# Kernel optimization log

Measured on AMD Instinct MI355X. Metric: run time of the kernel, lower is better.

## Reference

```python
import jax, jax.numpy as jnp
from jax import lax
import numpy as np

D = 128      # d_model
DI = 256     # d_inner = expand * d_model
NS = 16      # d_state
R = 8        # dt_rank = ceil(d_model/16)
DC = 4       # d_conv
B, C, N, P = 4, 32, 6, 64
T = N * P
RATIOS = (1, 3, 6)
OUT = 768


def _ln(x, g, b):
    m = x.mean(-1, keepdims=True)
    v = ((x - m) ** 2).mean(-1, keepdims=True)
    return (x - m) * lax.rsqrt(v + 1e-5) * g + b


def _event_order(n_base):
    # chronological interleaving of multi-band tokens (static, python-level)
    events = []
    for step in range(1, n_base + 1):
        for k, r in enumerate(RATIOS):
            if step % r == 0:
                events.append((k, step // r - 1))
    nk = [n_base // r for r in RATIOS]
    offs = np.cumsum([0] + nk[:-1])
    return np.array([offs[k] + w for k, w in events], dtype=np.int32)


def setup_inputs():
    key = jax.random.key(0)
    ks = iter(jax.random.split(key, 64))
    def nrm(shape, std):
        return jax.random.normal(next(ks), shape, jnp.float32) * std
    inp = {}
    inp['x'] = jax.random.normal(next(ks), (B, C, N, P), jnp.float32)
    inp['perm'] = jax.random.randint(next(ks), (B, C), 0, C)
    # sample_proj: Conv1d(1,D,7,pad=3) -> GELU -> Conv1d(D,D,1)
    inp['sp_w1'] = nrm((D, 1, 7), 0.3)
    inp['sp_b1'] = jnp.zeros((D,))
    inp['sp_w2'] = nrm((D, D, 1), D ** -0.5)
    inp['sp_b2'] = jnp.zeros((D,))
    nb = 4  # fwd0, fwd1, bwd0, bwd1 mamba blocks (stacked)
    inp['ln_g'] = jnp.ones((nb, D)); inp['ln_b'] = jnp.zeros((nb, D))
    inp['W_in'] = nrm((nb, D, 2 * DI), D ** -0.5)
    inp['conv_w'] = nrm((nb, DI, DC), DC ** -0.5)
    inp['conv_b'] = jnp.zeros((nb, DI))
    inp['W_x'] = nrm((nb, DI, R + 2 * NS), DI ** -0.5)
    inp['W_dt'] = nrm((nb, R, DI), R ** -0.5)
    inp['b_dt'] = jnp.full((nb, DI), -4.6) + nrm((nb, DI), 0.1)
    inp['A_log'] = jnp.broadcast_to(jnp.log(jnp.arange(1, NS + 1, dtype=jnp.float32)), (nb, DI, NS)) + 0.0
    inp['Dp'] = jnp.ones((nb, DI))
    inp['W_out'] = nrm((nb, DI, D), DI ** -0.5)
    inp['b_out'] = jnp.zeros((nb, D))
    inp['fuse_w'] = nrm((2 * D, D), (2 * D) ** -0.5); inp['fuse_b'] = jnp.zeros((D,))
    inp['band_emb'] = nrm((3, D), 0.02)
    inp['band_pw'] = nrm((3, D, D), D ** -0.5); inp['band_pb'] = jnp.zeros((3, D))
    inp['pos_w'] = nrm((D, 1, 19, 7), (19 * 7) ** -0.5); inp['pos_b'] = jnp.zeros((D,))
    inp['hemi_w'] = nrm((2 * D, D), (2 * D) ** -0.5); inp['hemi_b'] = jnp.zeros((D,))
    Lf = sum(N // r for r in RATIOS) * D  # flatten_dim = 9*128
    inp['a_ln_g'] = jnp.ones((Lf,)); inp['a_ln_b'] = jnp.zeros((Lf,))
    inp['a_w1'] = nrm((Lf, 200), Lf ** -0.5); inp['a_b1'] = jnp.zeros((200,))
    inp['a_w2'] = nrm((200, 1), 200 ** -0.5); inp['a_b2'] = jnp.zeros((1,))
    inp['m_ln_g'] = jnp.ones((Lf,)); inp['m_ln_b'] = jnp.zeros((Lf,))
    inp['m_w1'] = nrm((Lf, 1024), Lf ** -0.5); inp['m_b1'] = jnp.zeros((1024,))
    inp['m_w2'] = nrm((1024, OUT), 1024 ** -0.5); inp['m_b2'] = jnp.zeros((OUT,))
    return inp


def _mamba(h, lng, lnb, Win, cw, cb, Wx, Wdt, bdt, Alog, Dpar, Wout, bout):
    # pre-norm residual Mamba block: h + Mamba(LN(h))
    x = _ln(h, lng, lnb)
    xz = x @ Win                      # (BC,T,2*DI)
    xp, z = jnp.split(xz, 2, axis=-1)
    xt = xp.swapaxes(1, 2)            # (BC,DI,T)
    xt = lax.conv_general_dilated(xt, cw[:, None, :], (1,), [(DC - 1, 0)],
                                  dimension_numbers=('NCH', 'OIH', 'NCH'),
                                  feature_group_count=DI) + cb[None, :, None]
    xc = jax.nn.silu(xt).swapaxes(1, 2)   # (BC,T,DI)
    xdbl = xc @ Wx
    dt = jax.nn.softplus(xdbl[..., :R] @ Wdt + bdt)   # (BC,T,DI)
    Bs = xdbl[..., R:R + NS]
    Cs = xdbl[..., R + NS:]
    A = -jnp.exp(Alog)                # (DI,NS)
    def step(hc, inp):
        x_t, dt_t, b_t, c_t = inp
        hc = hc * jnp.exp(dt_t[..., None] * A) + (dt_t * x_t)[..., None] * b_t[:, None, :]
        return hc, jnp.einsum('bdn,bn->bd', hc, c_t)
    h0 = jnp.zeros((xc.shape[0], DI, NS), xc.dtype)
    _, ys = lax.scan(step, h0, (xc.swapaxes(0, 1), dt.swapaxes(0, 1),
                                Bs.swapaxes(0, 1), Cs.swapaxes(0, 1)))
    y = ys.swapaxes(0, 1) + xc * Dpar
    y = y * jax.nn.silu(z)
    return h + y @ Wout + bout


def reference(x, perm, sp_w1, sp_b1, sp_w2, sp_b2, ln_g, ln_b, W_in, conv_w, conv_b,
              W_x, W_dt, b_dt, A_log, Dp, W_out, b_out, fuse_w, fuse_b, band_emb,
              band_pw, band_pb, pos_w, pos_b, hemi_w, hemi_b, a_ln_g, a_ln_b,
              a_w1, a_b1, a_w2, a_b2, m_ln_g, m_ln_b, m_w1, m_b1, m_w2, m_b2):
    Bq, Cq, Nq, Pq = x.shape
    Tq = Nq * Pq
    ts = x.reshape(Bq * Cq, 1, Tq)
    # sample_proj
    f = lax.conv_general_dilated(ts, sp_w1, (1,), [(3, 3)],
                                 dimension_numbers=('NCH', 'OIH', 'NCH')) + sp_b1[None, :, None]
    f = jax.nn.gelu(f)
    f = jnp.einsum('bct,oc->bot', f, sp_w2[:, :, 0]) + sp_b2[None, :, None]
    h = f.swapaxes(1, 2)              # (BC,T,D)
    # bidirectional mamba stack
    hf = h
    for i in range(2):
        hf = _mamba(hf, ln_g[i], ln_b[i], W_in[i], conv_w[i], conv_b[i], W_x[i],
                    W_dt[i], b_dt[i], A_log[i], Dp[i], W_out[i], b_out[i])
    hb = h[:, ::-1]
    for i in range(2, 4):
        hb = _mamba(hb, ln_g[i], ln_b[i], W_in[i], conv_w[i], conv_b[i], W_x[i],
                    W_dt[i], b_dt[i], A_log[i], Dp[i], W_out[i], b_out[i])
    hb = hb[:, ::-1]
    feats = jnp.concatenate([hf, hb], -1) @ fuse_w + fuse_b   # (BC,T,D)
    # multi-band token extraction (end-of-period samples)
    band = []
    for k, r in enumerate(RATIOS):
        p = Pq * r
        nk = Tq // p
        pos = jnp.arange(nk) * p + (p - 1)
        band.append(feats[:, pos] @ band_pw[k] + band_pb[k] + band_emb[k])
    flat = jnp.concatenate(band, axis=1)
    toks = flat[:, jnp.asarray(_event_order(Nq))]   # chronological interleave, (BC,L,D)
    L = toks.shape[1]
    t = toks.reshape(Bq, Cq, L, D).transpose(0, 3, 1, 2)   # (B,D,C,L)
    pe = lax.conv_general_dilated(t, pos_w, (1, 1), [(9, 9), (3, 3)],
                                  dimension_numbers=('NCHW', 'OIHW', 'NCHW'),
                                  feature_group_count=D) + pos_b[None, :, None, None]
    t = (t + pe).transpose(0, 2, 3, 1)              # (B,C,L,D)
    # hemispheric channel gather + fuse
    tf = jnp.take_along_axis(t, perm[:, :, None, None], axis=1)
    fused = jnp.concatenate([t, tf], -1) @ hemi_w + hemi_b
    flatf = fused.reshape(Bq, Cq, L * D)
    # attention-MLP semantic readout
    logits = (jax.nn.gelu(_ln(flatf, a_ln_g, a_ln_b) @ a_w1 + a_b1) @ a_w2 + a_b2)[..., 0]
    w = jax.nn.softmax(logits, -1)
    agg = jnp.einsum('bcf,bc->bf', flatf, w)
    return jax.nn.gelu(_ln(agg, m_ln_g, m_ln_b) @ m_w1 + m_b1) @ m_w2 + m_b2
```

## Files before the change

kernel.cpp:

```cpp
#include <hip/hip_runtime.h>


typedef unsigned short u16;
using bf16x8 = __attribute__((ext_vector_type(8))) short;
using f32x4  = __attribute__((ext_vector_type(4))) float;

#define TT    384
#define BCn   128
#define TOKn  49152
#define CH3   64
#define NCH3  (TT/CH3)

__device__ __forceinline__ float b2f(u16 u) {
  return __uint_as_float(((unsigned)u) << 16);
}
__device__ __forceinline__ u16 f2b(float f) {
  unsigned u = __float_as_uint(f);
  u += 0x7fffu + ((u >> 16) & 1u);
  return (u16)(u >> 16);
}
__device__ __forceinline__ float gelu_t(float x) {
  float u2 = 1.5957691216057308f * (x + 0.044715f * x * x * x);
  float e = __expf(u2);
  float th = 1.f - 2.f / (e + 1.f);
  return 0.5f * x * (1.f + th);
}
__device__ __forceinline__ float silu_f(float x) { return x / (1.f + __expf(-x)); }
__device__ __forceinline__ float softplus_f(float x) {
  return fmaxf(x, 0.f) + __logf(1.f + __expf(-fabsf(x)));
}

__device__ __forceinline__ float dpp_xor1(float v) {
  return __int_as_float(__builtin_amdgcn_mov_dpp(
      __float_as_int(v), 0xB1 , 0xF, 0xF, true));
}
__device__ __forceinline__ float dpp_xor2(float v) {
  return __int_as_float(__builtin_amdgcn_mov_dpp(
      __float_as_int(v), 0x4E , 0xF, 0xF, true));
}

__device__ __forceinline__ float block_sum(float v, float* sb) {
  #pragma unroll
  for (int m = 32; m; m >>= 1) v += __shfl_xor(v, m);
  int lane = threadIdx.x & 63, wid = threadIdx.x >> 6;
  if (lane == 0) sb[wid] = v;
  __syncthreads();
  float tot = sb[0] + sb[1] + sb[2] + sb[3];
  __syncthreads();
  return tot;
}

template <int EPI, int KT>
__global__ __launch_bounds__(256) void k_mm(
    const u16* __restrict__ X, const u16* __restrict__ WT,
    const float* __restrict__ bias, int Nw, int rev,
    float* __restrict__ o0, u16* __restrict__ ob0) {
  constexpr int AK = KT + 8;
  __shared__ u16 As[64 * AK];
  __shared__ u16 Bs[64 * AK];
  const int tid = threadIdx.x;
  const int tok0 = blockIdx.x * 64;
  const int n0 = blockIdx.y * 64;

  constexpr int VPR = KT / 8;
  constexpr int ITER = 64 * VPR / 256;
  #pragma unroll
  for (int j = 0; j < ITER; ++j) {
    int idx = tid + j * 256;
    int row = idx / VPR, vec = idx % VPR;
    *reinterpret_cast<uint4*>(&As[row * AK + vec * 8]) =
        *reinterpret_cast<const uint4*>(&X[(size_t)(tok0 + row) * KT + vec * 8]);
    *reinterpret_cast<uint4*>(&Bs[row * AK + vec * 8]) =
        *reinterpret_cast<const uint4*>(&WT[(size_t)(n0 + row) * KT + vec * 8]);
  }
  __syncthreads();

  const int w = tid >> 6, lane = tid & 63;
  const int wm = (w & 1) * 32, wn = (w >> 1) * 32;
  const int lrow = lane & 15, quad = lane >> 4;
  f32x4 acc[2][2] = {};
  #pragma unroll
  for (int ks = 0; ks < KT / 32; ++ks) {
    int koff = ks * 32 + quad * 8;
    bf16x8 a0 = *reinterpret_cast<const bf16x8*>(&As[(wm + lrow) * AK + koff]);
    bf16x8 a1 = *reinterpret_cast<const bf16x8*>(&As[(wm + 16 + lrow) * AK + koff]);
    bf16x8 b0 = *reinterpret_cast<const bf16x8*>(&Bs[(wn + lrow) * AK + koff]);
    bf16x8 b1 = *reinterpret_cast<const bf16x8*>(&Bs[(wn + 16 + lrow) * AK + koff]);
    acc[0][0] = __builtin_amdgcn_mfma_f32_16x16x32_bf16(a0, b0, acc[0][0], 0, 0, 0);
    acc[0][1] = __builtin_amdgcn_mfma_f32_16x16x32_bf16(a0, b1, acc[0][1], 0, 0, 0);
    acc[1][0] = __builtin_amdgcn_mfma_f32_16x16x32_bf16(a1, b0, acc[1][0], 0, 0, 0);
    acc[1][1] = __builtin_amdgcn_mfma_f32_16x16x32_bf16(a1, b1, acc[1][1], 0, 0, 0);
  }

  #pragma unroll
  for (int mi = 0; mi < 2; ++mi)
    #pragma unroll
    for (int ni = 0; ni < 2; ++ni)
      #pragma unroll
      for (int r = 0; r < 4; ++r) {
        int tok = tok0 + wm + mi * 16 + quad * 4 + r;
        int n = n0 + wn + ni * 16 + lrow;
        float v = acc[mi][ni][r];
        if (EPI == 0) {
          v += bias[n];
          int bc = tok / TT, t = tok % TT;
          int tok2 = rev ? (bc * TT + (TT - 1 - t)) : tok;
          o0[(size_t)tok2 * 128 + n] = v;
        } else if (EPI == 1) {
          ob0[(size_t)tok * 512 + n] = f2b(v);
        } else if (EPI == 2) {
          if (n < 40) o0[(size_t)tok * 40 + n] = v;
        } else if (EPI == 3) {
          v += bias[n];
          o0[(size_t)tok * 128 + n] += v;
        }
      }
  (void)Nw;
}

__global__ __launch_bounds__(256) void k_tin(const float* __restrict__ W,
                                             u16* __restrict__ WT) {
  int i = blockIdx.x * 256 + threadIdx.x;
  int blk = i >> 16, r = i & 65535;
  int n = r >> 7, k = r & 127;
  WT[i] = f2b(W[blk * 65536 + k * 512 + n]);
}
__global__ __launch_bounds__(256) void k_tout(const float* __restrict__ W,
                                              u16* __restrict__ WT) {
  int i = blockIdx.x * 256 + threadIdx.x;
  int blk = i >> 15, r = i & 32767;
  int n = r >> 8, k = r & 255;
  WT[i] = f2b(W[blk * 32768 + k * 128 + n]);
}
__global__ __launch_bounds__(256) void k_tx(const float* __restrict__ W,
                                            u16* __restrict__ WT) {
  int i = blockIdx.x * 256 + threadIdx.x;
  int blk = i >> 14, r = i & 16383;
  int n = r >> 8, k = r & 255;
  WT[i] = (n < 40) ? f2b(W[blk * 10240 + k * 40 + n]) : 0;
}
__global__ __launch_bounds__(256) void k_tsp(const float* __restrict__ W,
                                             u16* __restrict__ WT) {
  int i = blockIdx.x * 256 + threadIdx.x;
  WT[i] = f2b(W[i]);
}

__global__ __launch_bounds__(256) void k_spec1(const float* __restrict__ x,
                                               const float* __restrict__ w1,
                                               const float* __restrict__ b1,
                                               u16* __restrict__ F) {
  __shared__ float xs[70];
  __shared__ float wsh[128 * 7];
  __shared__ float bs[128];
  int bc = blockIdx.x / 6, tile = blockIdx.x % 6;
  int tid = threadIdx.x;
  for (int i = tid; i < 896; i += 256) wsh[i] = w1[i];
  if (tid < 128) bs[tid] = b1[tid];
  int t0 = tile * 64;
  if (tid < 70) {
    int t = t0 - 3 + tid;
    xs[tid] = (t >= 0 && t < TT) ? x[(size_t)bc * TT + t] : 0.f;
  }
  __syncthreads();
  #pragma unroll
  for (int k = 0; k < 32; ++k) {
    int idx = tid + k * 256;
    int tl = idx >> 7, c = idx & 127;
    const float* wr = &wsh[c * 7];
    float acc = bs[c];
    #pragma unroll
    for (int j = 0; j < 7; ++j) acc += xs[tl + j] * wr[j];
    F[((size_t)(bc * TT + t0 + tl)) * 128 + c] = f2b(gelu_t(acc));
  }
}

__global__ __launch_bounds__(256) void k_ln(const float* __restrict__ H,
                                            const float* __restrict__ gg,
                                            const float* __restrict__ bb,
                                            u16* __restrict__ XLN) {
  int tid = threadIdx.x;
  int lane = tid & 63, wid = tid >> 6;
  int token = blockIdx.x * 4 + wid;
  const float* hr = H + (size_t)token * 128;
  float a = hr[lane], b = hr[lane + 64];
  float s = a + b;
  #pragma unroll
  for (int m = 32; m; m >>= 1) s += __shfl_xor(s, m);
  float mean = s * (1.f / 128.f);
  float d1 = a - mean, d2 = b - mean;
  float q = d1 * d1 + d2 * d2;
  #pragma unroll
  for (int m = 32; m; m >>= 1) q += __shfl_xor(q, m);
  float rs = rsqrtf(q * (1.f / 128.f) + 1e-5f);
  XLN[(size_t)token * 128 + lane] = f2b(d1 * rs * gg[lane] + bb[lane]);
  XLN[(size_t)token * 128 + lane + 64] =
      f2b(d2 * rs * gg[lane + 64] + bb[lane + 64]);
}

__global__ __launch_bounds__(256) void k_conv(const u16* __restrict__ XZ,
                                              const float* __restrict__ cw,
                                              const float* __restrict__ cb,
                                              u16* __restrict__ XC) {
  int idx = blockIdx.x * 256 + threadIdx.x;
  int d4 = idx & 63;
  int tokg = idx >> 6;
  int t = tokg % TT;
  int dbase = d4 * 4;
  const float* cwp = cw + dbase * 4;
  float wv[4][4];
  #pragma unroll
  for (int j = 0; j < 4; ++j)
    #pragma unroll
    for (int k = 0; k < 4; ++k) wv[j][k] = cwp[j * 4 + k];
  float accv[4];
  #pragma unroll
  for (int j = 0; j < 4; ++j) accv[j] = cb[dbase + j];
  #pragma unroll
  for (int k = 0; k < 4; ++k) {
    int tt = t + k - 3;
    if (tt < 0) continue;
    ushort4 xv = *reinterpret_cast<const ushort4*>(
        &XZ[(size_t)(tokg + k - 3) * 512 + dbase]);
    u16 xa[4];
    *reinterpret_cast<ushort4*>(xa) = xv;
    #pragma unroll
    for (int j = 0; j < 4; ++j) accv[j] += b2f(xa[j]) * wv[j][k];
  }
  u16 oa[4];
  #pragma unroll
  for (int j = 0; j < 4; ++j) oa[j] = f2b(silu_f(accv[j]));
  *reinterpret_cast<ushort4*>(&XC[(size_t)tokg * 256 + dbase]) =
      *reinterpret_cast<ushort4*>(oa);
}

__global__ __launch_bounds__(256) void k_scan(
    const float* __restrict__ XDBL, u16* __restrict__ XC,
    const u16* __restrict__ XZ, const float* __restrict__ Wdt,
    const float* __restrict__ bdt, const float* __restrict__ Alog,
    const float* __restrict__ Dpv) {
  __shared__ float xdl[CH3 * 40];
  __shared__ float dtl[CH3 * 64];
  __shared__ u16   xcl[CH3 * 64];
  __shared__ u16   ybuf[CH3 * 64];
  const int tid = threadIdx.x;
  const int bc = blockIdx.x >> 2, dq = blockIdx.x & 3;
  const int ng = tid & 3;
  const int dl = tid >> 2;
  const int dcol = tid & 63;

  const int d_scan = dq * 64 + dl;
  float A[4];
  #pragma unroll
  for (int j = 0; j < 4; ++j)
    A[j] = -__expf(Alog[d_scan * 16 + ng * 4 + j]);
  float wdtr[8];
  #pragma unroll
  for (int j = 0; j < 8; ++j) wdtr[j] = Wdt[j * 256 + dq * 64 + dcol];
  const float bd = bdt[dq * 64 + dcol];
  const float dpar = Dpv[dq * 64 + dcol];

  const size_t base = (size_t)bc * TT;
  const float* xdg = XDBL + base * 40;
  const uint4* xcu4 = (const uint4*)XC;

  float sx[10];
  uint4 scx[2];
  auto issue_loads = [&](int c) {
    const float* p = xdg + (size_t)c * CH3 * 40;
    #pragma unroll
    for (int k = 0; k < 10; ++k) sx[k] = p[tid + k * 256];
    #pragma unroll
    for (int k = 0; k < 2; ++k) {
      int v = tid + k * 256;
      int t = v >> 3, q = v & 7;
      size_t tok = base + (size_t)c * CH3 + t;
      scx[k] = xcu4[tok * 32 + dq * 8 + q];
    }
  };
  auto write_lds = [&]() {
    #pragma unroll
    for (int k = 0; k < 10; ++k) xdl[tid + k * 256] = sx[k];
    #pragma unroll
    for (int k = 0; k < 2; ++k) {
      int v = tid + k * 256;
      ((uint4*)xcl)[v] = scx[k];
    }
  };

  issue_loads(0);
  write_lds();
  __syncthreads();

  float hc[4] = {};
  for (int c = 0; c < NCH3; ++c) {
    if (c + 1 < NCH3) issue_loads(c + 1);
    #pragma unroll
    for (int k = 0; k < 16; ++k) {
      int t = (tid >> 6) + 4 * k;
      float4 x0 = *reinterpret_cast<const float4*>(&xdl[t * 40]);
      float4 x1 = *reinterpret_cast<const float4*>(&xdl[t * 40 + 4]);
      float acc = bd;
      acc += x0.x * wdtr[0] + x0.y * wdtr[1] + x0.z * wdtr[2] + x0.w * wdtr[3];
      acc += x1.x * wdtr[4] + x1.y * wdtr[5] + x1.z * wdtr[6] + x1.w * wdtr[7];
      dtl[t * 64 + dcol] = softplus_f(acc);
    }
    __syncthreads();
    #pragma unroll 4
    for (int t = 0; t < CH3; ++t) {
      float dtv = dtl[t * 64 + dl];
      float xcv = b2f(xcl[t * 64 + dl]);
      float4 Bv = *reinterpret_cast<const float4*>(&xdl[t * 40 + 8 + ng * 4]);
      float4 Cv = *reinterpret_cast<const float4*>(&xdl[t * 40 + 24 + ng * 4]);
      float dx = dtv * xcv;
      float e0 = __expf(A[0] * dtv);
      float e1 = __expf(A[1] * dtv);
      float e2 = __expf(A[2] * dtv);
      float e3 = __expf(A[3] * dtv);
      hc[0] = fmaf(hc[0], e0, dx * Bv.x);
      hc[1] = fmaf(hc[1], e1, dx * Bv.y);
      hc[2] = fmaf(hc[2], e2, dx * Bv.z);
      hc[3] = fmaf(hc[3], e3, dx * Bv.w);
      float yv = hc[0] * Cv.x + hc[1] * Cv.y + hc[2] * Cv.z + hc[3] * Cv.w;
      yv += dpp_xor1(yv);
      yv += dpp_xor2(yv);
      if (ng == 0) ybuf[t * 64 + dl] = f2b(yv);
    }
    __syncthreads();
    #pragma unroll
    for (int k = 0; k < 16; ++k) {
      int t = (tid >> 6) + 4 * k;
      int v = t * 64 + dcol;
      size_t tok = base + (size_t)c * CH3 + t;
      float y = b2f(ybuf[v]);
      float xcv = b2f(xcl[v]);
      float zz = b2f(XZ[tok * 512 + 256 + dq * 64 + dcol]);
      y = (y + xcv * dpar) * silu_f(zz);
      XC[tok * 256 + dq * 64 + dcol] = f2b(y);
    }
    __syncthreads();
    if (c + 1 < NCH3) {
      write_lds();
      __syncthreads();
    }
  }
}

__global__ __launch_bounds__(256) void k_gather(const float* __restrict__ H,
                                                float* __restrict__ XF,
                                                int half, int revpos) {
  int i = blockIdx.x * 256 + threadIdx.x;
  int col = i & 127, row = i >> 7;
  int bc = row / 6, u = row % 6;
  int tu = 63 + 64 * u;
  int t = revpos ? (TT - 1 - tu) : tu;
  XF[(size_t)row * 256 + half + col] = H[(size_t)(bc * TT + t) * 128 + col];
}

__global__ __launch_bounds__(128) void k_fuse(const float* __restrict__ XF,
                                              const float* __restrict__ fw,
                                              const float* __restrict__ fb,
                                              float* __restrict__ FE) {
  int row = blockIdx.x;
  int d = threadIdx.x;
  __shared__ float rows[256];
  rows[d] = XF[(size_t)row * 256 + d];
  rows[128 + d] = XF[(size_t)row * 256 + 128 + d];
  __syncthreads();
  float acc = fb[d];
  for (int k = 0; k < 256; ++k) acc += rows[k] * fw[k * 128 + d];
  FE[(size_t)row * 128 + d] = acc;
}

__global__ __launch_bounds__(128) void k_band(const float* __restrict__ FE,
                                              const float* __restrict__ pw,
                                              const float* __restrict__ pb,
                                              const float* __restrict__ pe,
                                              float* __restrict__ TO) {
  const int u_of[9] = {0, 1, 2, 2, 3, 4, 5, 5, 5};
  const int k_of[9] = {0, 0, 0, 1, 0, 0, 0, 1, 2};
  int bid = blockIdx.x;
  int bc = bid / 9, j = bid % 9;
  int u = u_of[j], kq = k_of[j];
  __shared__ float fs[128];
  int d = threadIdx.x;
  fs[d] = FE[(size_t)(bc * 6 + u) * 128 + d];
  __syncthreads();
  float acc = pb[kq * 128 + d] + pe[kq * 128 + d];
  const float* wp = pw + kq * 16384 + d;
  for (int c = 0; c < 128; ++c) acc += fs[c] * wp[c * 128];
  TO[(size_t)bid * 128 + d] = acc;
}

__global__ __launch_bounds__(256) void k_pos(const float* __restrict__ TO,
                                             const float* __restrict__ pw,
                                             const float* __restrict__ pb,
                                             float* __restrict__ T2) {
  int idx = blockIdx.x * 256 + threadIdx.x;
  int d = idx & 127;
  int l = (idx >> 7) % 9;
  int c = (idx / 1152) & 31;
  int b = idx / 36864;
  float acc = 0.f;
  const float* wd = pw + d * 133;
  for (int i = 0; i < 19; ++i) {
    int ci = c + i - 9;
    if (ci < 0 || ci >= 32) continue;
    const float* trow = TO + (size_t)(b * 32 + ci) * 9 * 128 + d;
    #pragma unroll
    for (int jj = 0; jj < 7; ++jj) {
      int lj = l + jj - 3;
      if (lj < 0 || lj >= 9) continue;
      acc += trow[lj * 128] * wd[i * 7 + jj];
    }
  }
  T2[idx] = TO[idx] + acc + pb[d];
}

__global__ __launch_bounds__(128) void k_hemi(const float* __restrict__ T2,
                                              const int* __restrict__ perm,
                                              const float* __restrict__ hw,
                                              const float* __restrict__ hb,
                                              float* __restrict__ FL) {
  int bid = blockIdx.x;
  int b = bid / 288;
  int c = (bid / 9) % 32;
  int l = bid % 9;
  int pc = perm[b * 32 + c];
  __shared__ float rows[256];
  int d = threadIdx.x;
  rows[d] = T2[((size_t)(b * 32 + c) * 9 + l) * 128 + d];
  rows[128 + d] = T2[((size_t)(b * 32 + pc) * 9 + l) * 128 + d];
  __syncthreads();
  float acc = hb[d];
  for (int k = 0; k < 256; ++k) acc += rows[k] * hw[k * 128 + d];
  FL[(size_t)(b * 32 + c) * 1152 + l * 128 + d] = acc;
}

__global__ __launch_bounds__(256) void k_attn(
    const float* __restrict__ FL, const float* __restrict__ lg,
    const float* __restrict__ lb, const float* __restrict__ w1,
    const float* __restrict__ b1, const float* __restrict__ w2,
    const float* __restrict__ ab2, float* __restrict__ LO) {
  __shared__ float xn[1152];
  __shared__ float sb[4];
  int row = blockIdx.x;
  int tid = threadIdx.x;
  const float* xr = FL + (size_t)row * 1152;
  float xl[5];
  int cnt = 0;
  float s = 0.f;
  for (int i = tid; i < 1152; i += 256) { xl[cnt] = xr[i]; s += xl[cnt]; ++cnt; }
  float tot = block_sum(s, sb);
  float mean = tot * (1.f / 1152.f);
  float q = 0.f;
  for (int k = 0; k < cnt; ++k) { float dd = xl[k] - mean; q += dd * dd; }
  float qt = block_sum(q, sb);
  float rs = rsqrtf(qt * (1.f / 1152.f) + 1e-5f);
  cnt = 0;
  for (int i = tid; i < 1152; i += 256) {
    xn[i] = (xl[cnt] - mean) * rs * lg[i] + lb[i];
    ++cnt;
  }
  __syncthreads();
  float g = 0.f;
  if (tid < 200) {
    float acc = b1[tid];
    for (int i = 0; i < 1152; ++i) acc += xn[i] * w1[i * 200 + tid];
    g = gelu_t(acc);
  }
  __syncthreads();
  if (tid < 200) xn[tid] = g;
  __syncthreads();
  float s2 = (tid < 200) ? xn[tid] * w2[tid] : 0.f;
  float t2 = block_sum(s2, sb);
  if (tid == 0) LO[row] = t2 + ab2[0];
}

__global__ __launch_bounds__(256) void k_smagg(const float* __restrict__ FL,
                                               const float* __restrict__ LO,
                                               float* __restrict__ AG) {
  int b = blockIdx.x;
  int tid = threadIdx.x;
  __shared__ float w[32];
  if (tid == 0) {
    float mx = -1e30f;
    for (int c = 0; c < 32; ++c) mx = fmaxf(mx, LO[b * 32 + c]);
    float sum = 0.f;
    for (int c = 0; c < 32; ++c) { float e = __expf(LO[b * 32 + c] - mx); w[c] = e; sum += e; }
    float inv = 1.f / sum;
    for (int c = 0; c < 32; ++c) w[c] *= inv;
  }
  __syncthreads();
  for (int f = tid; f < 1152; f += 256) {
    float acc = 0.f;
    for (int c = 0; c < 32; ++c) acc += FL[(size_t)(b * 32 + c) * 1152 + f] * w[c];
    AG[b * 1152 + f] = acc;
  }
}

__global__ __launch_bounds__(256) void k_lnm(const float* __restrict__ AG,
                                             const float* __restrict__ lg,
                                             const float* __restrict__ lb,
                                             float* __restrict__ AGN) {
  __shared__ float sb[4];
  int b = blockIdx.x;
  int tid = threadIdx.x;
  const float* xr = AG + b * 1152;
  float xl[5];
  int cnt = 0;
  float s = 0.f;
  for (int i = tid; i < 1152; i += 256) { xl[cnt] = xr[i]; s += xl[cnt]; ++cnt; }
  float tot = block_sum(s, sb);
  float mean = tot * (1.f / 1152.f);
  float q = 0.f;
  for (int k = 0; k < cnt; ++k) { float dd = xl[k] - mean; q += dd * dd; }
  float qt = block_sum(q, sb);
  float rs = rsqrtf(qt * (1.f / 1152.f) + 1e-5f);
  cnt = 0;
  for (int i = tid; i < 1152; i += 256) {
    AGN[b * 1152 + i] = (xl[cnt] - mean) * rs * lg[i] + lb[i];
    ++cnt;
  }
}

__global__ __launch_bounds__(256) void k_g1(const float* __restrict__ AGN,
                                            const float* __restrict__ w1,
                                            const float* __restrict__ b1,
                                            float* __restrict__ G1) {
  int b = blockIdx.y;
  int j = blockIdx.x * 256 + threadIdx.x;
  __shared__ float av[1152];
  for (int i = threadIdx.x; i < 1152; i += 256) av[i] = AGN[b * 1152 + i];
  __syncthreads();
  float acc = b1[j];
  for (int i = 0; i < 1152; ++i) acc += av[i] * w1[(size_t)i * 1024 + j];
  G1[b * 1024 + j] = gelu_t(acc);
}

__global__ __launch_bounds__(256) void k_f3(const float* __restrict__ G1,
                                            const float* __restrict__ w2,
                                            const float* __restrict__ b2v,
                                            float* __restrict__ out) {
  int b = blockIdx.y;
  int o = blockIdx.x * 256 + threadIdx.x;
  __shared__ float gv[1024];
  for (int i = threadIdx.x; i < 1024; i += 256) gv[i] = G1[b * 1024 + i];
  __syncthreads();
  float acc = b2v[o];
  for (int i = 0; i < 1024; ++i) acc += gv[i] * w2[(size_t)i * 768 + o];
  out[b * 768 + o] = acc;
}

extern "C" void kernel_launch(void* const* d_in, const int* in_sizes, int n_in,
                              void* d_out, int out_size, void* d_ws,
                              size_t ws_size, hipStream_t stream) {
  (void)in_sizes; (void)n_in; (void)out_size; (void)ws_size;
  const float* x      = (const float*)d_in[0];
  const int*   perm   = (const int*)d_in[1];
  const float* sp_w1  = (const float*)d_in[2];
  const float* sp_b1  = (const float*)d_in[3];
  const float* sp_w2  = (const float*)d_in[4];
  const float* sp_b2  = (const float*)d_in[5];
  const float* ln_g   = (const float*)d_in[6];
  const float* ln_b   = (const float*)d_in[7];
  const float* W_in   = (const float*)d_in[8];
  const float* conv_w = (const float*)d_in[9];
  const float* conv_b = (const float*)d_in[10];
  const float* W_x    = (const float*)d_in[11];
  const float* W_dt   = (const float*)d_in[12];
  const float* b_dt   = (const float*)d_in[13];
  const float* A_log  = (const float*)d_in[14];
  const float* Dp     = (const float*)d_in[15];
  const float* W_out  = (const float*)d_in[16];
  const float* b_out  = (const float*)d_in[17];
  const float* fuse_w = (const float*)d_in[18];
  const float* fuse_b = (const float*)d_in[19];
  const float* band_emb = (const float*)d_in[20];
  const float* band_pw  = (const float*)d_in[21];
  const float* band_pb  = (const float*)d_in[22];
  const float* pos_w  = (const float*)d_in[23];
  const float* pos_b  = (const float*)d_in[24];
  const float* hemi_w = (const float*)d_in[25];
  const float* hemi_b = (const float*)d_in[26];
  const float* a_ln_g = (const float*)d_in[27];
  const float* a_ln_b = (const float*)d_in[28];
  const float* a_w1   = (const float*)d_in[29];
  const float* a_b1   = (const float*)d_in[30];
  const float* a_w2   = (const float*)d_in[31];
  const float* a_b2   = (const float*)d_in[32];
  const float* m_ln_g = (const float*)d_in[33];
  const float* m_ln_b = (const float*)d_in[34];
  const float* m_w1   = (const float*)d_in[35];
  const float* m_b1   = (const float*)d_in[36];
  const float* m_w2   = (const float*)d_in[37];
  const float* m_b2   = (const float*)d_in[38];

  char* ws = (char*)d_ws;
  size_t off = 0;
  auto alloc = [&](size_t bytes) -> char* {
    char* p = ws + off;
    off += (bytes + 255) & ~(size_t)255;
    return p;
  };
  float* H    = (float*)alloc((size_t)TOKn * 128 * 4);
  u16*   F    = (u16*)  alloc((size_t)TOKn * 128 * 2);
  u16*   XLN  = (u16*)  alloc((size_t)TOKn * 128 * 2);
  u16*   XZ   = (u16*)  alloc((size_t)TOKn * 512 * 2);
  u16*   XC   = (u16*)  alloc((size_t)TOKn * 256 * 2);
  float* XDBL = (float*)alloc((size_t)TOKn * 40 * 4);
  u16*   WTin = (u16*)alloc(4 * 512 * 128 * 2);
  u16*   WTout= (u16*)alloc(4 * 128 * 256 * 2);
  u16*   WTx  = (u16*)alloc(4 * 64 * 256 * 2);
  u16*   WTsp = (u16*)alloc(128 * 128 * 2);
  float* XF   = (float*)alloc(768 * 256 * 4);
  float* FE   = (float*)alloc(768 * 128 * 4);
  float* TO   = (float*)alloc(1152 * 128 * 4);
  float* T2v  = (float*)alloc(147456 * 4);
  float* FL   = (float*)alloc(147456 * 4);
  float* LO   = (float*)alloc(128 * 4);
  float* AG   = (float*)alloc(4 * 1152 * 4);
  float* AGN  = (float*)alloc(4 * 1152 * 4);
  float* G1v  = (float*)alloc(4 * 1024 * 4);

  k_tin <<<dim3(1024), dim3(256), 0, stream>>>(W_in, WTin);
  k_tout<<<dim3(512),  dim3(256), 0, stream>>>(W_out, WTout);
  k_tx  <<<dim3(256),  dim3(256), 0, stream>>>(W_x, WTx);
  k_tsp <<<dim3(64),   dim3(256), 0, stream>>>(sp_w2, WTsp);

  k_spec1<<<dim3(BCn * 6), dim3(256), 0, stream>>>(x, sp_w1, sp_b1, F);

  auto mamba_round = [&](int blk) {
    k_ln<<<dim3(TOKn / 4), dim3(256), 0, stream>>>(
        H, ln_g + blk * 128, ln_b + blk * 128, XLN);
    k_mm<1, 128><<<dim3(TOKn / 64, 8), dim3(256), 0, stream>>>(
        XLN, WTin + (size_t)blk * 65536, nullptr, 512, 0, nullptr, XZ);
    k_conv<<<dim3(TOKn * 64 / 256), dim3(256), 0, stream>>>(
        XZ, conv_w + blk * 1024, conv_b + blk * 256, XC);
    k_mm<2, 256><<<dim3(TOKn / 64, 1), dim3(256), 0, stream>>>(
        XC, WTx + (size_t)blk * 16384, nullptr, 40, 0, XDBL, nullptr);
    k_scan<<<dim3(BCn * 4), dim3(256), 0, stream>>>(
        XDBL, XC, XZ, W_dt + blk * 2048, b_dt + blk * 256,
        A_log + blk * 4096, Dp + blk * 256);
    k_mm<3, 256><<<dim3(TOKn / 64, 2), dim3(256), 0, stream>>>(
        XC, WTout + (size_t)blk * 32768, b_out + blk * 128, 128, 0,
        H, nullptr);
  };

  k_mm<0, 128><<<dim3(TOKn / 64, 2), dim3(256), 0, stream>>>(
      F, WTsp, sp_b2, 128, 0, H, nullptr);
  mamba_round(0);
  mamba_round(1);
  k_gather<<<dim3(384), dim3(256), 0, stream>>>(H, XF, 0, 0);

  k_mm<0, 128><<<dim3(TOKn / 64, 2), dim3(256), 0, stream>>>(
      F, WTsp, sp_b2, 128, 1, H, nullptr);
  mamba_round(2);
  mamba_round(3);
  k_gather<<<dim3(384), dim3(256), 0, stream>>>(H, XF, 128, 1);

  k_fuse<<<dim3(768), dim3(128), 0, stream>>>(XF, fuse_w, fuse_b, FE);
  k_band<<<dim3(1152), dim3(128), 0, stream>>>(FE, band_pw, band_pb, band_emb, TO);
  k_pos<<<dim3(576), dim3(256), 0, stream>>>(TO, pos_w, pos_b, T2v);
  k_hemi<<<dim3(1152), dim3(128), 0, stream>>>(T2v, perm, hemi_w, hemi_b, FL);
  k_attn<<<dim3(128), dim3(256), 0, stream>>>(FL, a_ln_g, a_ln_b, a_w1, a_b1,
                                              a_w2, a_b2, LO);
  k_smagg<<<dim3(4), dim3(256), 0, stream>>>(FL, LO, AG);
  k_lnm<<<dim3(4), dim3(256), 0, stream>>>(AG, m_ln_g, m_ln_b, AGN);
  k_g1<<<dim3(4, 4), dim3(256), 0, stream>>>(AGN, m_w1, m_b1, G1v);
  k_f3<<<dim3(3, 4), dim3(256), 0, stream>>>(G1v, m_w2, m_b2, (float*)d_out);
}
```

Baseline: 1.119 ms.

## Batch forward and backward Mamba directions into merged launches

Processes the forward and backward Mamba stacks together by doubling the token dimension, so each launch selects per-half weights and halves the number of kernel launches per layer. The two halves run concurrently, which roughly doubles the grid size; the scan kernel in particular moves from 512 to 1024 blocks. The four weight-transpose kernels are merged into one, and the scan's bf16 y buffer is replaced by reusing the dt shared buffer in fp32. In exchange it needs about twice the workspace and falls back to the old sequential path when the workspace is too small.

```diff
diff --git a/kernel.cpp b/kernel.cpp
--- a/kernel.cpp
+++ b/kernel.cpp
@@ -52,8 +52,9 @@
 
 template <int EPI, int KT>
 __global__ __launch_bounds__(256) void k_mm(
-    const u16* __restrict__ X, const u16* __restrict__ WT,
-    const float* __restrict__ bias, int Nw, int rev,
+    const u16* __restrict__ X, const u16* __restrict__ WT0,
+    const u16* __restrict__ WT1, const float* __restrict__ bias0,
+    const float* __restrict__ bias1, int rev,
     float* __restrict__ o0, u16* __restrict__ ob0) {
   constexpr int AK = KT + 8;
   __shared__ u16 As[64 * AK];
@@ -61,6 +62,9 @@
   const int tid = threadIdx.x;
   const int tok0 = blockIdx.x * 64;
   const int n0 = blockIdx.y * 64;
+  const bool hi = (tok0 >= TOKn);
+  const u16* __restrict__ WT = hi ? WT1 : WT0;
+  const float* __restrict__ bias = hi ? bias1 : bias0;
 
   constexpr int VPR = KT / 8;
   constexpr int ITER = 64 * VPR / 256;
@@ -68,8 +72,10 @@
   for (int j = 0; j < ITER; ++j) {
     int idx = tid + j * 256;
     int row = idx / VPR, vec = idx % VPR;
+    int srow = tok0 + row;
+    if (EPI == 0 && srow >= TOKn) srow -= TOKn;
     *reinterpret_cast<uint4*>(&As[row * AK + vec * 8]) =
-        *reinterpret_cast<const uint4*>(&X[(size_t)(tok0 + row) * KT + vec * 8]);
+        *reinterpret_cast<const uint4*>(&X[(size_t)srow * KT + vec * 8]);
     *reinterpret_cast<uint4*>(&Bs[row * AK + vec * 8]) =
         *reinterpret_cast<const uint4*>(&WT[(size_t)(n0 + row) * KT + vec * 8]);
   }
@@ -103,9 +109,12 @@
         float v = acc[mi][ni][r];
         if (EPI == 0) {
           v += bias[n];
-          int bc = tok / TT, t = tok % TT;
-          int tok2 = rev ? (bc * TT + (TT - 1 - t)) : tok;
-          o0[(size_t)tok2 * 128 + n] = v;
+          int tl = tok, off = 0;
+          if (tok >= TOKn) { tl -= TOKn; off = TOKn; }
+          int bc = tl / TT, t = tl % TT;
+          bool dorev = (rev == 1) || (rev == 2 && off != 0);
+          int t2 = dorev ? (TT - 1 - t) : t;
+          o0[(size_t)(off + bc * TT + t2) * 128 + n] = v;
         } else if (EPI == 1) {
           ob0[(size_t)tok * 512 + n] = f2b(v);
         } else if (EPI == 2) {
@@ -115,34 +124,32 @@
           o0[(size_t)tok * 128 + n] += v;
         }
       }
-  (void)Nw;
-}
-
-__global__ __launch_bounds__(256) void k_tin(const float* __restrict__ W,
-                                             u16* __restrict__ WT) {
+}
+
+__global__ __launch_bounds__(256) void k_tw(
+    const float* __restrict__ Win, const float* __restrict__ Wout,
+    const float* __restrict__ Wx, const float* __restrict__ Wsp,
+    u16* __restrict__ Tin, u16* __restrict__ Tout,
+    u16* __restrict__ Tx, u16* __restrict__ Tsp) {
   int i = blockIdx.x * 256 + threadIdx.x;
-  int blk = i >> 16, r = i & 65535;
-  int n = r >> 7, k = r & 127;
-  WT[i] = f2b(W[blk * 65536 + k * 512 + n]);
-}
-__global__ __launch_bounds__(256) void k_tout(const float* __restrict__ W,
-                                              u16* __restrict__ WT) {
-  int i = blockIdx.x * 256 + threadIdx.x;
-  int blk = i >> 15, r = i & 32767;
-  int n = r >> 8, k = r & 255;
-  WT[i] = f2b(W[blk * 32768 + k * 128 + n]);
-}
-__global__ __launch_bounds__(256) void k_tx(const float* __restrict__ W,
-                                            u16* __restrict__ WT) {
-  int i = blockIdx.x * 256 + threadIdx.x;
-  int blk = i >> 14, r = i & 16383;
-  int n = r >> 8, k = r & 255;
-  WT[i] = (n < 40) ? f2b(W[blk * 10240 + k * 40 + n]) : 0;
-}
-__global__ __launch_bounds__(256) void k_tsp(const float* __restrict__ W,
-                                             u16* __restrict__ WT) {
-  int i = blockIdx.x * 256 + threadIdx.x;
-  WT[i] = f2b(W[i]);
+  if (i < 262144) {
+    int blk = i >> 16, r = i & 65535;
+    int n = r >> 7, k = r & 127;
+    Tin[i] = f2b(Win[blk * 65536 + k * 512 + n]);
+  } else if (i < 393216) {
+    int j = i - 262144;
+    int blk = j >> 15, r = j & 32767;
+    int n = r >> 8, k = r & 255;
+    Tout[j] = f2b(Wout[blk * 32768 + k * 128 + n]);
+  } else if (i < 458752) {
+    int j = i - 393216;
+    int blk = j >> 14, r = j & 16383;
+    int n = r >> 8, k = r & 255;
+    Tx[j] = (n < 40) ? f2b(Wx[blk * 10240 + k * 40 + n]) : (u16)0;
+  } else if (i < 475136) {
+    int j = i - 458752;
+    Tsp[j] = f2b(Wsp[j]);
+  }
 }
 
 __global__ __launch_bounds__(256) void k_spec1(const float* __restrict__ x,
@@ -175,12 +182,16 @@
 }
 
 __global__ __launch_bounds__(256) void k_ln(const float* __restrict__ H,
-                                            const float* __restrict__ gg,
-                                            const float* __restrict__ bb,
+                                            const float* __restrict__ g0,
+                                            const float* __restrict__ b0,
+                                            const float* __restrict__ g1,
+                                            const float* __restrict__ b1,
                                             u16* __restrict__ XLN) {
   int tid = threadIdx.x;
   int lane = tid & 63, wid = tid >> 6;
   int token = blockIdx.x * 4 + wid;
+  const float* gg = (token >= TOKn) ? g1 : g0;
+  const float* bb = (token >= TOKn) ? b1 : b0;
   const float* hr = H + (size_t)token * 128;
   float a = hr[lane], b = hr[lane + 64];
   float s = a + b;
@@ -198,14 +209,18 @@
 }
 
 __global__ __launch_bounds__(256) void k_conv(const u16* __restrict__ XZ,
-                                              const float* __restrict__ cw,
-                                              const float* __restrict__ cb,
+                                              const float* __restrict__ cw0,
+                                              const float* __restrict__ cb0,
+                                              const float* __restrict__ cw1,
+                                              const float* __restrict__ cb1,
                                               u16* __restrict__ XC) {
   int idx = blockIdx.x * 256 + threadIdx.x;
   int d4 = idx & 63;
   int tokg = idx >> 6;
   int t = tokg % TT;
   int dbase = d4 * 4;
+  const float* cw = (tokg >= TOKn) ? cw1 : cw0;
+  const float* cb = (tokg >= TOKn) ? cb1 : cb0;
   const float* cwp = cw + dbase * 4;
   float wv[4][4];
   #pragma unroll
@@ -235,15 +250,21 @@
 
 __global__ __launch_bounds__(256) void k_scan(
     const float* __restrict__ XDBL, u16* __restrict__ XC,
-    const u16* __restrict__ XZ, const float* __restrict__ Wdt,
-    const float* __restrict__ bdt, const float* __restrict__ Alog,
-    const float* __restrict__ Dpv) {
+    const u16* __restrict__ XZ,
+    const float* __restrict__ Wdt0, const float* __restrict__ bdt0,
+    const float* __restrict__ Alog0, const float* __restrict__ Dpv0,
+    const float* __restrict__ Wdt1, const float* __restrict__ bdt1,
+    const float* __restrict__ Alog1, const float* __restrict__ Dpv1) {
   __shared__ float xdl[CH3 * 40];
   __shared__ float dtl[CH3 * 64];
   __shared__ u16   xcl[CH3 * 64];
-  __shared__ u16   ybuf[CH3 * 64];
   const int tid = threadIdx.x;
   const int bc = blockIdx.x >> 2, dq = blockIdx.x & 3;
+  const bool hi = (bc >= BCn);
+  const float* __restrict__ Wdt  = hi ? Wdt1  : Wdt0;
+  const float* __restrict__ bdt  = hi ? bdt1  : bdt0;
+  const float* __restrict__ Alog = hi ? Alog1 : Alog0;
+  const float* __restrict__ Dpv  = hi ? Dpv1  : Dpv0;
   const int ng = tid & 3;
   const int dl = tid >> 2;
   const int dcol = tid & 63;
@@ -323,7 +344,7 @@
       float yv = hc[0] * Cv.x + hc[1] * Cv.y + hc[2] * Cv.z + hc[3] * Cv.w;
       yv += dpp_xor1(yv);
       yv += dpp_xor2(yv);
-      if (ng == 0) ybuf[t * 64 + dl] = f2b(yv);
+      if (ng == 0) dtl[t * 64 + dl] = yv;
     }
     __syncthreads();
     #pragma unroll
@@ -331,7 +352,7 @@
       int t = (tid >> 6) + 4 * k;
       int v = t * 64 + dcol;
       size_t tok = base + (size_t)c * CH3 + t;
-      float y = b2f(ybuf[v]);
+      float y = dtl[v];
       float xcv = b2f(xcl[v]);
       float zz = b2f(XZ[tok * 512 + 256 + dq * 64 + dcol]);
       y = (y + xcv * dpar) * silu_f(zz);
@@ -554,7 +575,7 @@
 extern "C" void kernel_launch(void* const* d_in, const int* in_sizes, int n_in,
                               void* d_out, int out_size, void* d_ws,
                               size_t ws_size, hipStream_t stream) {
-  (void)in_sizes; (void)n_in; (void)out_size; (void)ws_size;
+  (void)in_sizes; (void)n_in; (void)out_size;
   const float* x      = (const float*)d_in[0];
   const int*   perm   = (const int*)d_in[1];
   const float* sp_w1  = (const float*)d_in[2];
@@ -595,6 +616,23 @@
   const float* m_w2   = (const float*)d_in[37];
   const float* m_b2   = (const float*)d_in[38];
 
+  size_t need = 0;
+  {
+    auto a = [&](size_t b) { need += (b + 255) & ~(size_t)255; };
+    a((size_t)2 * TOKn * 128 * 4);
+    a((size_t)2 * TOKn * 128 * 2);
+    a((size_t)2 * TOKn * 512 * 2);
+    a((size_t)2 * TOKn * 256 * 2);
+    a((size_t)2 * TOKn * 40 * 4);
+    a(4 * 512 * 128 * 2); a(4 * 128 * 256 * 2); a(4 * 64 * 256 * 2);
+    a(128 * 128 * 2);
+    a(768 * 256 * 4); a(768 * 128 * 4); a(1152 * 128 * 4);
+    a(147456 * 4); a(147456 * 4);
+    a(128 * 4); a(4 * 1152 * 4); a(4 * 1152 * 4); a(4 * 1024 * 4);
+  }
+  const bool merged = ws_size >= need;
+  const int NTOT = merged ? 2 * TOKn : TOKn;
+
   char* ws = (char*)d_ws;
   size_t off = 0;
   auto alloc = [&](size_t bytes) -> char* {
@@ -602,12 +640,12 @@
     off += (bytes + 255) & ~(size_t)255;
     return p;
   };
-  float* H    = (float*)alloc((size_t)TOKn * 128 * 4);
-  u16*   F    = (u16*)  alloc((size_t)TOKn * 128 * 2);
-  u16*   XLN  = (u16*)  alloc((size_t)TOKn * 128 * 2);
-  u16*   XZ   = (u16*)  alloc((size_t)TOKn * 512 * 2);
-  u16*   XC   = (u16*)  alloc((size_t)TOKn * 256 * 2);
-  float* XDBL = (float*)alloc((size_t)TOKn * 40 * 4);
+  float* H    = (float*)alloc((size_t)NTOT * 128 * 4);
+  u16*   XLN  = (u16*)  alloc((size_t)NTOT * 128 * 2);
+  u16*   F    = merged ? XLN : (u16*)alloc((size_t)TOKn * 128 * 2);
+  u16*   XZ   = (u16*)  alloc((size_t)NTOT * 512 * 2);
+  u16*   XC   = (u16*)  alloc((size_t)NTOT * 256 * 2);
+  float* XDBL = (float*)alloc((size_t)NTOT * 40 * 4);
   u16*   WTin = (u16*)alloc(4 * 512 * 128 * 2);
   u16*   WTout= (u16*)alloc(4 * 128 * 256 * 2);
   u16*   WTx  = (u16*)alloc(4 * 64 * 256 * 2);
@@ -622,41 +660,53 @@
   float* AGN  = (float*)alloc(4 * 1152 * 4);
   float* G1v  = (float*)alloc(4 * 1024 * 4);
 
-  k_tin <<<dim3(1024), dim3(256), 0, stream>>>(W_in, WTin);
-  k_tout<<<dim3(512),  dim3(256), 0, stream>>>(W_out, WTout);
-  k_tx  <<<dim3(256),  dim3(256), 0, stream>>>(W_x, WTx);
-  k_tsp <<<dim3(64),   dim3(256), 0, stream>>>(sp_w2, WTsp);
+  k_tw<<<dim3(1856), dim3(256), 0, stream>>>(W_in, W_out, W_x, sp_w2,
+                                             WTin, WTout, WTx, WTsp);
 
   k_spec1<<<dim3(BCn * 6), dim3(256), 0, stream>>>(x, sp_w1, sp_b1, F);
 
-  auto mamba_round = [&](int blk) {
-    k_ln<<<dim3(TOKn / 4), dim3(256), 0, stream>>>(
-        H, ln_g + blk * 128, ln_b + blk * 128, XLN);
-    k_mm<1, 128><<<dim3(TOKn / 64, 8), dim3(256), 0, stream>>>(
-        XLN, WTin + (size_t)blk * 65536, nullptr, 512, 0, nullptr, XZ);
-    k_conv<<<dim3(TOKn * 64 / 256), dim3(256), 0, stream>>>(
-        XZ, conv_w + blk * 1024, conv_b + blk * 256, XC);
-    k_mm<2, 256><<<dim3(TOKn / 64, 1), dim3(256), 0, stream>>>(
-        XC, WTx + (size_t)blk * 16384, nullptr, 40, 0, XDBL, nullptr);
-    k_scan<<<dim3(BCn * 4), dim3(256), 0, stream>>>(
-        XDBL, XC, XZ, W_dt + blk * 2048, b_dt + blk * 256,
-        A_log + blk * 4096, Dp + blk * 256);
-    k_mm<3, 256><<<dim3(TOKn / 64, 2), dim3(256), 0, stream>>>(
-        XC, WTout + (size_t)blk * 32768, b_out + blk * 128, 128, 0,
-        H, nullptr);
+  auto mamba_round = [&](int lo, int hi) {
+    k_ln<<<dim3(NTOT / 4), dim3(256), 0, stream>>>(
+        H, ln_g + lo * 128, ln_b + lo * 128,
+        ln_g + hi * 128, ln_b + hi * 128, XLN);
+    k_mm<1, 128><<<dim3(NTOT / 64, 8), dim3(256), 0, stream>>>(
+        XLN, WTin + (size_t)lo * 65536, WTin + (size_t)hi * 65536,
+        nullptr, nullptr, 0, nullptr, XZ);
+    k_conv<<<dim3(NTOT * 64 / 256), dim3(256), 0, stream>>>(
+        XZ, conv_w + lo * 1024, conv_b + lo * 256,
+        conv_w + hi * 1024, conv_b + hi * 256, XC);
+    k_mm<2, 256><<<dim3(NTOT / 64, 1), dim3(256), 0, stream>>>(
+        XC, WTx + (size_t)lo * 16384, WTx + (size_t)hi * 16384,
+        nullptr, nullptr, 0, XDBL, nullptr);
+    k_scan<<<dim3((NTOT / TT) * 4), dim3(256), 0, stream>>>(
+        XDBL, XC, XZ,
+        W_dt + lo * 2048, b_dt + lo * 256, A_log + lo * 4096, Dp + lo * 256,
+        W_dt + hi * 2048, b_dt + hi * 256, A_log + hi * 4096, Dp + hi * 256);
+    k_mm<3, 256><<<dim3(NTOT / 64, 2), dim3(256), 0, stream>>>(
+        XC, WTout + (size_t)lo * 32768, WTout + (size_t)hi * 32768,
+        b_out + lo * 128, b_out + hi * 128, 0, H, nullptr);
   };
 
-  k_mm<0, 128><<<dim3(TOKn / 64, 2), dim3(256), 0, stream>>>(
-      F, WTsp, sp_b2, 128, 0, H, nullptr);
-  mamba_round(0);
-  mamba_round(1);
-  k_gather<<<dim3(384), dim3(256), 0, stream>>>(H, XF, 0, 0);
-
-  k_mm<0, 128><<<dim3(TOKn / 64, 2), dim3(256), 0, stream>>>(
-      F, WTsp, sp_b2, 128, 1, H, nullptr);
-  mamba_round(2);
-  mamba_round(3);
-  k_gather<<<dim3(384), dim3(256), 0, stream>>>(H, XF, 128, 1);
+  if (merged) {
+    k_mm<0, 128><<<dim3(NTOT / 64, 2), dim3(256), 0, stream>>>(
+        F, WTsp, WTsp, sp_b2, sp_b2, 2, H, nullptr);
+    mamba_round(0, 2);
+    mamba_round(1, 3);
+    k_gather<<<dim3(384), dim3(256), 0, stream>>>(H, XF, 0, 0);
+    k_gather<<<dim3(384), dim3(256), 0, stream>>>(
+        H + (size_t)TOKn * 128, XF, 128, 1);
+  } else {
+    k_mm<0, 128><<<dim3(NTOT / 64, 2), dim3(256), 0, stream>>>(
+        F, WTsp, WTsp, sp_b2, sp_b2, 0, H, nullptr);
+    mamba_round(0, 0);
+    mamba_round(1, 1);
+    k_gather<<<dim3(384), dim3(256), 0, stream>>>(H, XF, 0, 0);
+    k_mm<0, 128><<<dim3(NTOT / 64, 2), dim3(256), 0, stream>>>(
+        F, WTsp, WTsp, sp_b2, sp_b2, 1, H, nullptr);
+    mamba_round(2, 2);
+    mamba_round(3, 3);
+    k_gather<<<dim3(384), dim3(256), 0, stream>>>(H, XF, 128, 1);
+  }
 
   k_fuse<<<dim3(768), dim3(128), 0, stream>>>(XF, fuse_w, fuse_b, FE);
   k_band<<<dim3(1152), dim3(128), 0, stream>>>(FE, band_pw, band_pb, band_emb, TO);
```

After: 1.129 ms. No clear change (+0.9%).
